# Optimization experiments

Hardware: AMD Instinct MI355X
Metric: run time of the kernel (lower is better)

Reference implementation:

```python
import jax, jax.numpy as jnp
import numpy as np

ROWS, COLS, DIM, BATCH = 128, 128, 64, 128

def setup_inputs() -> dict:
    key = jax.random.key(0)
    kx, kw = jax.random.split(key)
    x = jax.random.normal(kx, (BATCH, DIM), dtype=jnp.float32)
    # SOM codebook weights, randomly initialized as in _initialize_weights()
    weights = jax.random.normal(kw, (ROWS, COLS, DIM), dtype=jnp.float32)
    return {"x": x, "weights": weights}

def reference(x, weights):
    # Squared Euclidean distance from each input to every grid neuron.
    # x: (B, D); weights: (R, C, D) -> distances: (B, R, C)
    diff = weights[None, :, :, :] - x[:, None, None, :]
    distances = jnp.sum(diff * diff, axis=-1)
    return distances
```

## Files before the change

kernel.cpp:

```cpp
#include <hip/hip_runtime.h>


#define SOM_B   128
#define SOM_D   64
#define SOM_N   16384
#define SOM_BT  16
#define SOM_TPB 256

__global__ __launch_bounds__(SOM_TPB)
void som_prep(const float* __restrict__ x,
              const float* __restrict__ w,
              float4* __restrict__ wt,
              float* __restrict__ x2) {
    const int tid = threadIdx.x;
    const int j   = blockIdx.x * SOM_TPB + tid;
    const int i   = j >> 14;
    const int n   = j & (SOM_N - 1);
    const float4* w4 = (const float4*)w;
    wt[j] = w4[(n << 4) | i];

    if (blockIdx.x < SOM_B && tid < 64) {
        float v = x[(blockIdx.x << 6) + tid];
        float s = v * v;
        #pragma unroll
        for (int off = 32; off > 0; off >>= 1)
            s += __shfl_down(s, off, 64);
        if (tid == 0) x2[blockIdx.x] = s;
    }
}

__global__ __launch_bounds__(SOM_TPB, 2)
void som_main(const float* __restrict__ x,
              const float4* __restrict__ wt,
              const float* __restrict__ x2,
              float* __restrict__ out) {
    const int tid = threadIdx.x;
    const int n   = blockIdx.x * SOM_TPB + tid;
    const int b0  = blockIdx.y * SOM_BT;

    float4 wr[16];
    #pragma unroll
    for (int i = 0; i < 16; ++i) wr[i] = wt[(i << 14) + n];

    float wn2 = 0.f;
    #pragma unroll
    for (int i = 0; i < 16; ++i)
        wn2 += wr[i].x * wr[i].x + wr[i].y * wr[i].y
             + wr[i].z * wr[i].z + wr[i].w * wr[i].w;

    const float4* x4 = (const float4*)x;
    float* op = out + (size_t)b0 * SOM_N + n;

    #pragma unroll
    for (int b = 0; b < SOM_BT; ++b) {
        const float4* xb = x4 + ((b0 + b) << 4);
        float a0 = 0.f, a1 = 0.f, a2 = 0.f, a3 = 0.f;
        #pragma unroll
        for (int i = 0; i < 16; i += 4) {
            float4 xv0 = xb[i + 0];
            float4 xv1 = xb[i + 1];
            float4 xv2 = xb[i + 2];
            float4 xv3 = xb[i + 3];
            a0 += wr[i + 0].x * xv0.x + wr[i + 0].y * xv0.y
                + wr[i + 0].z * xv0.z + wr[i + 0].w * xv0.w;
            a1 += wr[i + 1].x * xv1.x + wr[i + 1].y * xv1.y
                + wr[i + 1].z * xv1.z + wr[i + 1].w * xv1.w;
            a2 += wr[i + 2].x * xv2.x + wr[i + 2].y * xv2.y
                + wr[i + 2].z * xv2.z + wr[i + 2].w * xv2.w;
            a3 += wr[i + 3].x * xv3.x + wr[i + 3].y * xv3.y
                + wr[i + 3].z * xv3.z + wr[i + 3].w * xv3.w;
        }
        float acc = (a0 + a1) + (a2 + a3);
        op[(size_t)b * SOM_N] = fmaf(-2.f, acc, wn2 + x2[b0 + b]);
    }
}

extern "C" void kernel_launch(void* const* d_in, const int* in_sizes, int n_in,
                              void* d_out, int out_size, void* d_ws, size_t ws_size,
                              hipStream_t stream) {
    const float* x = (const float*)d_in[0];
    const float* w = (const float*)d_in[1];
    float* out = (float*)d_out;

    float4* wt = (float4*)d_ws;
    float*  x2 = (float*)((char*)d_ws + SOM_N * SOM_D * 4);

    som_prep<<<dim3((SOM_N * SOM_D / 4) / SOM_TPB), dim3(SOM_TPB), 0, stream>>>(x, w, wt, x2);
    som_main<<<dim3(SOM_N / SOM_TPB, SOM_B / SOM_BT), dim3(SOM_TPB), 0, stream>>>(x, wt, x2, out);
}
```

Before: 77.33 us.

## Fuse prep and distance kernels, reading weights directly without transpose

New measurement: 71.76 us. 1.08x faster.

```diff
diff --git a/kernel.cpp b/kernel.cpp
--- a/kernel.cpp
+++ b/kernel.cpp
@@ -7,40 +7,38 @@
 #define SOM_BT  16
 #define SOM_TPB 256
 
-__global__ __launch_bounds__(SOM_TPB)
-void som_prep(const float* __restrict__ x,
-              const float* __restrict__ w,
-              float4* __restrict__ wt,
-              float* __restrict__ x2) {
-    const int tid = threadIdx.x;
-    const int j   = blockIdx.x * SOM_TPB + tid;
-    const int i   = j >> 14;
-    const int n   = j & (SOM_N - 1);
-    const float4* w4 = (const float4*)w;
-    wt[j] = w4[(n << 4) | i];
+__global__ __launch_bounds__(SOM_TPB, 2)
+void som_dist_kernel(const float* __restrict__ x,
+                     const float* __restrict__ w,
+                     float* __restrict__ out) {
+    __shared__ float x2s[SOM_BT];
 
-    if (blockIdx.x < SOM_B && tid < 64) {
-        float v = x[(blockIdx.x << 6) + tid];
-        float s = v * v;
-        #pragma unroll
-        for (int off = 32; off > 0; off >>= 1)
-            s += __shfl_down(s, off, 64);
-        if (tid == 0) x2[blockIdx.x] = s;
-    }
-}
-
-__global__ __launch_bounds__(SOM_TPB, 2)
-void som_main(const float* __restrict__ x,
-              const float4* __restrict__ wt,
-              const float* __restrict__ x2,
-              float* __restrict__ out) {
     const int tid = threadIdx.x;
     const int n   = blockIdx.x * SOM_TPB + tid;
     const int b0  = blockIdx.y * SOM_BT;
 
+    const float4* x4 = (const float4*)x;
+
     float4 wr[16];
-    #pragma unroll
-    for (int i = 0; i < 16; ++i) wr[i] = wt[(i << 14) + n];
+    {
+        const float4* wg = (const float4*)(w + (size_t)n * SOM_D);
+        #pragma unroll
+        for (int i = 0; i < 16; ++i) wr[i] = wg[i];
+    }
+
+    if (tid < SOM_BT) {
+        const float4* xr = x4 + ((b0 + tid) << 4);
+        float s0 = 0.f, s1 = 0.f, s2 = 0.f, s3 = 0.f;
+        #pragma unroll
+        for (int i = 0; i < 16; i += 4) {
+            float4 v0 = xr[i + 0], v1 = xr[i + 1], v2 = xr[i + 2], v3 = xr[i + 3];
+            s0 += v0.x * v0.x + v0.y * v0.y + v0.z * v0.z + v0.w * v0.w;
+            s1 += v1.x * v1.x + v1.y * v1.y + v1.z * v1.z + v1.w * v1.w;
+            s2 += v2.x * v2.x + v2.y * v2.y + v2.z * v2.z + v2.w * v2.w;
+            s3 += v3.x * v3.x + v3.y * v3.y + v3.z * v3.z + v3.w * v3.w;
+        }
+        x2s[tid] = (s0 + s1) + (s2 + s3);
+    }
 
     float wn2 = 0.f;
     #pragma unroll
@@ -48,7 +46,8 @@
         wn2 += wr[i].x * wr[i].x + wr[i].y * wr[i].y
              + wr[i].z * wr[i].z + wr[i].w * wr[i].w;
 
-    const float4* x4 = (const float4*)x;
+    __syncthreads();
+
     float* op = out + (size_t)b0 * SOM_N + n;
 
     #pragma unroll
@@ -71,7 +70,7 @@
                 + wr[i + 3].z * xv3.z + wr[i + 3].w * xv3.w;
         }
         float acc = (a0 + a1) + (a2 + a3);
-        op[(size_t)b * SOM_N] = fmaf(-2.f, acc, wn2 + x2[b0 + b]);
+        op[(size_t)b * SOM_N] = fmaf(-2.f, acc, wn2 + x2s[b]);
     }
 }
 
@@ -82,9 +81,7 @@
     const float* w = (const float*)d_in[1];
     float* out = (float*)d_out;
 
-    float4* wt = (float4*)d_ws;
-    float*  x2 = (float*)((char*)d_ws + SOM_N * SOM_D * 4);
-
-    som_prep<<<dim3((SOM_N * SOM_D / 4) / SOM_TPB), dim3(SOM_TPB), 0, stream>>>(x, w, wt, x2);
-    som_main<<<dim3(SOM_N / SOM_TPB, SOM_B / SOM_BT), dim3(SOM_TPB), 0, stream>>>(x, wt, x2, out);
+    dim3 grid(SOM_N / SOM_TPB, SOM_B / SOM_BT);
+    dim3 block(SOM_TPB);
+    som_dist_kernel<<<grid, block, 0, stream>>>(x, w, out);
 }
```
